# Kernel tuning notes

Measured on AMD Instinct MI355X. Metric: run time of the kernel, lower is better.

## Reference

```python
import jax, jax.numpy as jnp
from jax import lax
import numpy as np

B, C, N, T, K = 16, 64, 512, 64, 2
KSIZE, DIL = 2, 1
PAD = (KSIZE - 1) * DIL
EPS = 1e-5


def _powers(A, k):
    Ps = [jnp.eye(A.shape[0], dtype=A.dtype)]
    for _ in range(k):
        Ps.append(Ps[-1] @ A)
    return jnp.stack(Ps)  # (K+1, N, N)


def setup_inputs() -> dict:
    key = jax.random.key(0)
    ks = jax.random.split(key, 12)
    x = jax.random.normal(ks[0], (B, C, N, T), dtype=jnp.float32)
    # row-normalized random transition matrices, precomputed powers
    Af = jax.random.uniform(ks[1], (N, N), dtype=jnp.float32)
    Af = Af / Af.sum(axis=1, keepdims=True)
    Ab = Af.T / Af.T.sum(axis=1, keepdims=True)
    Aa = jax.random.uniform(ks[2], (N, N), dtype=jnp.float32)
    Aa = Aa / Aa.sum(axis=1, keepdims=True)
    P_f_pows = _powers(Af, K)
    P_b_pows = _powers(Ab, K)
    A_adp_pows = _powers(Aa, K)
    s = 0.05
    filter_w = jax.random.normal(ks[3], (C, C, 1, KSIZE), dtype=jnp.float32) * s
    filter_b = jnp.zeros((C,), jnp.float32)
    gate_w = jax.random.normal(ks[4], (C, C, 1, KSIZE), dtype=jnp.float32) * s
    gate_b = jnp.zeros((C,), jnp.float32)
    skip_w = jax.random.normal(ks[5], (C, C, 1, 1), dtype=jnp.float32) * s
    skip_b = jnp.zeros((C,), jnp.float32)
    weight_f = jax.random.normal(ks[6], (K + 1, C, C), dtype=jnp.float32) * s
    weight_b = jax.random.normal(ks[7], (K + 1, C, C), dtype=jnp.float32) * s
    gcn_bias = jnp.zeros((C,), jnp.float32)
    ln_gamma = jnp.ones((C,), jnp.float32)
    ln_beta = jnp.zeros((C,), jnp.float32)
    alpha = jnp.float32(0.5)
    return dict(x=x, P_f_pows=P_f_pows, P_b_pows=P_b_pows, A_adp_pows=A_adp_pows,
                filter_w=filter_w, filter_b=filter_b, gate_w=gate_w, gate_b=gate_b,
                skip_w=skip_w, skip_b=skip_b, weight_f=weight_f, weight_b=weight_b,
                gcn_bias=gcn_bias, ln_gamma=ln_gamma, ln_beta=ln_beta, alpha=alpha)


def _conv(x, w, b, dil=1):
    y = lax.conv_general_dilated(x, w, window_strides=(1, 1), padding='VALID',
                                 rhs_dilation=(1, dil),
                                 dimension_numbers=('NCHW', 'OIHW', 'NCHW'))
    return y + b[None, :, None, None]


def _apply_powers(xt, P_pows, weights):
    # xt: (B*T, N, Cin); P_pows: (K+1, N, N); weights: (K+1, Cin, Cout)
    xk = jnp.einsum('kij,bjc->kbic', P_pows, xt)
    return jnp.einsum('kbic,kco->bio', xk, weights)


def reference(x, P_f_pows, P_b_pows, A_adp_pows,
              filter_w, filter_b, gate_w, gate_b, skip_w, skip_b,
              weight_f, weight_b, gcn_bias, ln_gamma, ln_beta, alpha):
    # --- Gated TCN (causal left-pad along time) ---
    x_pad = jnp.pad(x, ((0, 0), (0, 0), (0, 0), (PAD, 0)))
    f = jnp.tanh(_conv(x_pad, filter_w, filter_b, DIL))
    g = jax.nn.sigmoid(_conv(x_pad, gate_w, gate_b, DIL))
    out = f * g                                   # (B, C, N, T)
    skip = _conv(out, skip_w, skip_b)             # 1x1 conv
    x_temporal = x + out                          # in_channels == out_channels

    # --- Diffusion GCN on (B*T, N, C) ---
    xt = jnp.transpose(x_temporal, (0, 3, 2, 1)).reshape(B * T, N, C)
    static_out = (_apply_powers(xt, P_f_pows, weight_f)
                  + _apply_powers(xt, P_b_pows, weight_b)
                  + gcn_bias[None, None, :])
    adapt_out = (_apply_powers(xt, A_adp_pows, weight_f)
                 + _apply_powers(xt, A_adp_pows, weight_b)
                 + gcn_bias[None, None, :])

    a = jax.nn.sigmoid(alpha)
    x_gcn = a * static_out + (1.0 - a) * adapt_out

    # --- LayerNorm over channel dim (dropout = identity in eval) ---
    mu = x_gcn.mean(axis=-1, keepdims=True)
    var = ((x_gcn - mu) ** 2).mean(axis=-1, keepdims=True)
    x_gcn = (x_gcn - mu) * lax.rsqrt(var + EPS) * ln_gamma + ln_beta

    x_out = x_gcn.reshape(B, T, N, C).transpose(0, 3, 2, 1)  # (B, C, N, T)
    return (x_out, skip)
```

## Files before the change

kernel.cpp:

```cpp
#include <hip/hip_runtime.h>
#include <cstdint>
#include <cstddef>

#define NB 16
#define NC 64
#define NN 512
#define NT 64
#define BT (NB*NT)
#define NN2 (NN*NN)
#define XSTRIDE_B (NC*NN*NT)
#define XSTRIDE_C (NN*NT)
#define XT_ROW (BT*NC)

typedef __attribute__((ext_vector_type(8))) short short8;
typedef __attribute__((ext_vector_type(4))) float f32x4;
typedef unsigned short ushort_t;
typedef unsigned int uint_t;

__device__ __forceinline__ ushort_t f2bf(float f) {
    uint_t u = __builtin_bit_cast(uint_t, f);
    u += 0x7FFFu + ((u >> 16) & 1u);
    return (ushort_t)(u >> 16);
}
__device__ __forceinline__ float bf2f(ushort_t u) {
    return __builtin_bit_cast(float, (uint_t)u << 16);
}
__device__ __forceinline__ void gl_lds16(const void* g, void* s) {
    __builtin_amdgcn_global_load_lds(
        (const __attribute__((address_space(1))) unsigned int*)g,
        (__attribute__((address_space(3))) unsigned int*)s, 16, 0, 0);
}
__device__ __forceinline__ void wait_vm(int n) {
    if (n >= 7)      asm volatile("s_waitcnt vmcnt(7)" ::: "memory");
    else if (n == 5) asm volatile("s_waitcnt vmcnt(5)" ::: "memory");
    else if (n == 4) asm volatile("s_waitcnt vmcnt(4)" ::: "memory");
    else if (n == 3) asm volatile("s_waitcnt vmcnt(3)" ::: "memory");
    else if (n == 2) asm volatile("s_waitcnt vmcnt(2)" ::: "memory");
    else             asm volatile("s_waitcnt vmcnt(0)" ::: "memory");
}

__global__ void k_prep(const float* __restrict__ wf, const float* __restrict__ wb,
                       const float* __restrict__ alpha, ushort_t* __restrict__ Wcb) {
    int i = blockIdx.x * 256 + threadIdx.x;
    if (i >= 7 * 4096) return;
    float a = 1.f / (1.f + expf(-alpha[0]));
    int r = i >> 12, co = i & 4095;
    int c = co >> 6, o = co & 63;
    float v;
    if      (r == 0) v = wf[co] + wb[co];
    else if (r == 1) v = a * wf[4096 + co];
    else if (r == 2) v = a * wf[8192 + co];
    else if (r == 3) v = a * wb[4096 + co];
    else if (r == 4) v = a * wb[8192 + co];
    else if (r == 5) v = (1.f - a) * (wf[4096 + co] + wb[4096 + co]);
    else             v = (1.f - a) * (wf[8192 + co] + wb[8192 + co]);
    int chunk = ((c >> 5) << 2) | (o >> 4);
    int lane  = (((c >> 3) & 3) << 4) | (o & 15);
    int j     = c & 7;
    Wcb[r * 4096 + chunk * 512 + lane * 8 + j] = f2bf(v);
}

__global__ void k_prepP(const float* __restrict__ Pf, const float* __restrict__ Pb,
                        const float* __restrict__ Aa, ushort_t* __restrict__ Apk) {
    int i = blockIdx.x * 256 + threadIdx.x;
    if (i >= 196608) return;
    int lane = i & 63, kc = (i >> 6) & 15, nt = (i >> 10) & 31, r = i >> 15;
    const float* base;
    if      (r == 0) base = Pf + NN2;
    else if (r == 1) base = Pf + 2 * NN2;
    else if (r == 2) base = Pb + NN2;
    else if (r == 3) base = Pb + 2 * NN2;
    else if (r == 4) base = Aa + NN2;
    else             base = Aa + 2 * NN2;
    int n = nt * 16 + (lane & 15);
    int k0 = kc * 32 + (lane >> 4) * 8;
    const float* src = base + (size_t)n * NN + k0;
    float4 v0 = ((const float4*)src)[0];
    float4 v1 = ((const float4*)src)[1];
    uint4 o;
    o.x = (uint_t)f2bf(v0.x) | ((uint_t)f2bf(v0.y) << 16);
    o.y = (uint_t)f2bf(v0.z) | ((uint_t)f2bf(v0.w) << 16);
    o.z = (uint_t)f2bf(v1.x) | ((uint_t)f2bf(v1.y) << 16);
    o.w = (uint_t)f2bf(v1.z) | ((uint_t)f2bf(v1.w) << 16);
    *(uint4*)(Apk + (size_t)i * 8) = o;
}

__global__ void k_prepW(const float* __restrict__ fw, const float* __restrict__ gw,
                        const float* __restrict__ sw, ushort_t* __restrict__ Wt) {
    int i = blockIdx.x * 256 + threadIdx.x;
    if (i >= 5 * 4096) return;
    int mat = i >> 12, t = i & 4095;
    int chunk = t >> 9, l = (t >> 3) & 63, j = t & 7;
    int m = chunk >> 1, kb = chunk & 1;
    int o = m * 16 + (l & 15);
    int c = kb * 32 + ((l >> 4) << 3) + j;
    float v;
    if      (mat == 0) v = fw[o * 128 + c * 2 + 0];
    else if (mat == 1) v = fw[o * 128 + c * 2 + 1];
    else if (mat == 2) v = gw[o * 128 + c * 2 + 0];
    else if (mat == 3) v = gw[o * 128 + c * 2 + 1];
    else               v = sw[o * 64 + c];
    Wt[i] = f2bf(v);
}

#define XS_P 72
__device__ __forceinline__ int swzA(int r, int c) {
    return r * XS_P + (c ^ (((r >> 4) & 3) << 3));
}
__global__ __launch_bounds__(256, 3) void k_tcn(
    const float* __restrict__ x,
    const ushort_t* __restrict__ Wt,
    const float* __restrict__ fb, const float* __restrict__ gb,
    const float* __restrict__ sb,
    float* __restrict__ skip_out, ushort_t* __restrict__ XTbf) {
    __shared__ __align__(16) ushort_t Xs[65 * XS_P];
    __shared__ __align__(16) ushort_t Os[64 * XS_P];

    int tx = threadIdx.x;
    int b = blockIdx.x >> 9, n = blockIdx.x & (NN - 1);

    {
        int c = tx >> 2, tq = tx & 3, t0 = tq * 16;
        const float* src = x + (size_t)b * XSTRIDE_B + (size_t)c * XSTRIDE_C
                             + (size_t)n * NT + t0;
        float4 v0 = ((const float4*)src)[0];
        float4 v1 = ((const float4*)src)[1];
        float4 v2 = ((const float4*)src)[2];
        float4 v3 = ((const float4*)src)[3];
        float vv[16] = {v0.x, v0.y, v0.z, v0.w, v1.x, v1.y, v1.z, v1.w,
                        v2.x, v2.y, v2.z, v2.w, v3.x, v3.y, v3.z, v3.w};
#pragma unroll
        for (int e = 0; e < 16; ++e) {
            int r = t0 + e + 1;
            Xs[swzA(r, c)] = f2bf(vv[e]);
        }
        if (tx < 8) ((uint4*)Xs)[tx] = (uint4){0, 0, 0, 0};
    }
    __syncthreads();

    int w = tx >> 6, l = tx & 63, lr = l & 15, lg = l >> 4;

    short8 wf0[2], wf1[2], wg0[2], wg1[2], wsk[2];
#pragma unroll
    for (int kb = 0; kb < 2; ++kb) {
        int off = (w * 2 + kb) * 512 + l * 8;
        wf0[kb] = *(const short8*)(Wt + 0 * 4096 + off);
        wf1[kb] = *(const short8*)(Wt + 1 * 4096 + off);
        wg0[kb] = *(const short8*)(Wt + 2 * 4096 + off);
        wg1[kb] = *(const short8*)(Wt + 3 * 4096 + off);
        wsk[kb] = *(const short8*)(Wt + 4 * 4096 + off);
    }
    float fbv[4], gbv[4], sbv[4];
#pragma unroll
    for (int q = 0; q < 4; ++q) {
        int o = w * 16 + lg * 4 + q;
        fbv[q] = fb[o]; gbv[q] = gb[o]; sbv[q] = sb[o];
    }

#pragma unroll
    for (int tb = 0; tb < 4; ++tb) {
        short8 b0[2], b1[2];
#pragma unroll
        for (int kb = 0; kb < 2; ++kb) {
            int blk = kb * 4 + lg;
            int r1 = tb * 16 + lr + 1, r0 = tb * 16 + lr;
            b1[kb] = *(const short8*)&Xs[r1 * XS_P + (((blk ^ ((r1 >> 4) & 3)) << 3))];
            b0[kb] = *(const short8*)&Xs[r0 * XS_P + (((blk ^ ((r0 >> 4) & 3)) << 3))];
        }
        f32x4 aF = {fbv[0], fbv[1], fbv[2], fbv[3]};
        f32x4 aG = {gbv[0], gbv[1], gbv[2], gbv[3]};
        aF = __builtin_amdgcn_mfma_f32_16x16x32_bf16(wf0[0], b0[0], aF, 0, 0, 0);
        aF = __builtin_amdgcn_mfma_f32_16x16x32_bf16(wf0[1], b0[1], aF, 0, 0, 0);
        aF = __builtin_amdgcn_mfma_f32_16x16x32_bf16(wf1[0], b1[0], aF, 0, 0, 0);
        aF = __builtin_amdgcn_mfma_f32_16x16x32_bf16(wf1[1], b1[1], aF, 0, 0, 0);
        aG = __builtin_amdgcn_mfma_f32_16x16x32_bf16(wg0[0], b0[0], aG, 0, 0, 0);
        aG = __builtin_amdgcn_mfma_f32_16x16x32_bf16(wg0[1], b0[1], aG, 0, 0, 0);
        aG = __builtin_amdgcn_mfma_f32_16x16x32_bf16(wg1[0], b1[0], aG, 0, 0, 0);
        aG = __builtin_amdgcn_mfma_f32_16x16x32_bf16(wg1[1], b1[1], aG, 0, 0, 0);
        int t = tb * 16 + lr;
#pragma unroll
        for (int q = 0; q < 4; ++q) {
            float fo = tanhf(aF[q]);
            float go = 1.f / (1.f + expf(-aG[q]));
            int o = w * 16 + lg * 4 + q;
            Os[swzA(t, o)] = f2bf(fo * go);
        }
    }
    __syncthreads();

    float* skp = skip_out + (size_t)b * XSTRIDE_B + (size_t)n * NT;
#pragma unroll
    for (int tb = 0; tb < 4; ++tb) {
        int t = tb * 16 + lr;
        short8 ov[2];
#pragma unroll
        for (int kb = 0; kb < 2; ++kb) {
            int blk = kb * 4 + lg;
            ov[kb] = *(const short8*)&Os[t * XS_P + (((blk ^ ((t >> 4) & 3)) << 3))];
        }
        f32x4 aS = {sbv[0], sbv[1], sbv[2], sbv[3]};
        aS = __builtin_amdgcn_mfma_f32_16x16x32_bf16(wsk[0], ov[0], aS, 0, 0, 0);
        aS = __builtin_amdgcn_mfma_f32_16x16x32_bf16(wsk[1], ov[1], aS, 0, 0, 0);
#pragma unroll
        for (int q = 0; q < 4; ++q) {
            int o = w * 16 + lg * 4 + q;
            skp[(size_t)o * XSTRIDE_C + t] = aS[q];
        }
    }

    {
        int t = tx >> 2, cch = (tx & 3) * 16;
        ushort_t* dst = XTbf + (size_t)n * XT_ROW + (size_t)b * 4096 + t * 64 + cch;
        int rX = t + 1;
#pragma unroll
        for (int blk2 = 0; blk2 < 2; ++blk2) {
            int cb = (cch >> 3) + blk2;
            short8 xv = *(const short8*)&Xs[rX * XS_P + ((cb ^ ((rX >> 4) & 3)) << 3)];
            short8 ovv = *(const short8*)&Os[t * XS_P + ((cb ^ ((t >> 4) & 3)) << 3)];
            uint_t pk[4];
#pragma unroll
            for (int h = 0; h < 4; ++h) {
                float s0 = bf2f((ushort_t)xv[h * 2]) + bf2f((ushort_t)ovv[h * 2]);
                float s1 = bf2f((ushort_t)xv[h * 2 + 1]) + bf2f((ushort_t)ovv[h * 2 + 1]);
                pk[h] = (uint_t)f2bf(s0) | ((uint_t)f2bf(s1) << 16);
            }
            *(uint4*)(dst + blk2 * 8) = (uint4){pk[0], pk[1], pk[2], pk[3]};
        }
    }
}

__global__ __launch_bounds__(256) void k_tr(const ushort_t* __restrict__ XTbf,
                                            ushort_t* __restrict__ Bpk) {
    __shared__ ushort_t tile[32 * XS_P];
    int tx = threadIdx.x;
    int bt = blockIdx.x;
    int jj = tx >> 3, c8 = (tx & 7) * 8;
    int f = tx >> 6, lane = tx & 63, lg = lane >> 4, lr = lane & 15;
    for (int kc = 0; kc < 16; ++kc) {
        if (kc) __syncthreads();
        *(uint4*)&tile[jj * XS_P + c8] =
            *(const uint4*)(XTbf + (size_t)(kc * 32 + jj) * XT_ROW + bt * 64 + c8);
        __syncthreads();
        ushort_t vals[8];
#pragma unroll
        for (int e = 0; e < 8; ++e)
            vals[e] = tile[(lg * 8 + e) * XS_P + f * 16 + lr];
        uint4 o;
        o.x = (uint_t)vals[0] | ((uint_t)vals[1] << 16);
        o.y = (uint_t)vals[2] | ((uint_t)vals[3] << 16);
        o.z = (uint_t)vals[4] | ((uint_t)vals[5] << 16);
        o.w = (uint_t)vals[6] | ((uint_t)vals[7] << 16);
        *(uint4*)(Bpk + (size_t)bt * 32768 + kc * 2048 + tx * 8) = o;
    }
}

__global__ __launch_bounds__(256, 4) void k_gcn(
    const ushort_t* __restrict__ Apk,
    const ushort_t* __restrict__ Bpk,
    const ushort_t* __restrict__ XTbf,
    const ushort_t* __restrict__ Wcb,
    const float* __restrict__ bias,
    ushort_t* __restrict__ G) {
    __shared__ __align__(16) char smem[24576];

    int tx = threadIdx.x;
    int w = tx >> 6, l = tx & 63;
    int lr = l & 15, lg = l >> 4;
    int s = w >> 1, h = w & 1;

    int bid = (blockIdx.x & 7) * 2048 + (blockIdx.x >> 3);
    int bt = bid >> 4;
    int n0i = bid & 15;
    int n0 = n0i << 5;

    f32x4 acc[3][4];
#pragma unroll
    for (int j = 0; j < 3; ++j)
#pragma unroll
        for (int f = 0; f < 4; ++f) acc[j][f] = (f32x4){0.f, 0.f, 0.f, 0.f};

    const ushort_t* aBase = Apk + (size_t)(h * 3) * NN2
                                + (size_t)(n0i * 2 + s) * 8192 + l * 8;
    const ushort_t* a2Src = aBase + 2 * (size_t)NN2;
    const ushort_t* bSrc = Bpk + (size_t)bt * 32768 + w * 512 + l * 8;

    short8 aE[2], aO[2];
    aE[0] = *(const short8*)(aBase);
    aE[1] = *(const short8*)(aBase + NN2);
#pragma unroll
    for (int d = 0; d < 2; ++d)
        gl_lds16(a2Src + d * 512, smem + 16384 + d * 4096 + w * 1024);
#pragma unroll
    for (int d = 0; d < 3; ++d)
        gl_lds16(bSrc + d * 2048, smem + d * 4096 + w * 1024);
    wait_vm(2);
    __builtin_amdgcn_s_barrier();
    __builtin_amdgcn_sched_barrier(0);

#pragma unroll
    for (int t = 0; t < 16; ++t) {
        if (t + 1 < 16) {
            if ((t & 1) == 0) {
                aO[0] = *(const short8*)(aBase + (t + 1) * 512);
                aO[1] = *(const short8*)(aBase + NN2 + (t + 1) * 512);
            } else {
                aE[0] = *(const short8*)(aBase + (t + 1) * 512);
                aE[1] = *(const short8*)(aBase + NN2 + (t + 1) * 512);
            }
        }
        if (t + 2 < 16)
            gl_lds16(a2Src + (t + 2) * 512,
                     smem + 16384 + ((t + 2) & 1) * 4096 + w * 1024);
        if (t + 3 < 16)
            gl_lds16(bSrc + (t + 3) * 2048,
                     smem + ((t + 3) & 3) * 4096 + w * 1024);

        const char* sBr = smem + (t & 3) * 4096;
        short8 a2 = *(const short8*)(smem + 16384 + (t & 1) * 4096 + w * 1024 + l * 16);
        short8 bv[4];
#pragma unroll
        for (int f = 0; f < 4; ++f)
            bv[f] = *(const short8*)(sBr + f * 1024 + l * 16);

        __builtin_amdgcn_s_setprio(1);
        const short8 a0 = (t & 1) ? aO[0] : aE[0];
        const short8 a1 = (t & 1) ? aO[1] : aE[1];
#pragma unroll
        for (int f = 0; f < 4; ++f)
            acc[0][f] = __builtin_amdgcn_mfma_f32_16x16x32_bf16(a0, bv[f], acc[0][f], 0, 0, 0);
#pragma unroll
        for (int f = 0; f < 4; ++f)
            acc[1][f] = __builtin_amdgcn_mfma_f32_16x16x32_bf16(a1, bv[f], acc[1][f], 0, 0, 0);
#pragma unroll
        for (int f = 0; f < 4; ++f)
            acc[2][f] = __builtin_amdgcn_mfma_f32_16x16x32_bf16(a2, bv[f], acc[2][f], 0, 0, 0);
        __builtin_amdgcn_s_setprio(0);

        wait_vm(t <= 12 ? 5 : (t == 13 ? 4 : (t == 14 ? 2 : 0)));
        __builtin_amdgcn_s_barrier();
        __builtin_amdgcn_sched_barrier(0);
    }

    float* sC = (float*)smem;
    ushort_t* sYw = (ushort_t*)(smem + 8192) + w * 1152;

    f32x4 acc2[4];
#pragma unroll
    for (int fo = 0; fo < 4; ++fo) {
        float b = (h == 0) ? bias[fo * 16 + lr] : 0.f;
        acc2[fo] = (f32x4){b, b, b, b};
    }
    const ushort_t* wBase = Wcb + l * 8;

    if (h == 0) {
        const ushort_t* xs = XTbf + (size_t)(n0 + s * 16 + lr) * XT_ROW + bt * 64 + lg * 8;
        short8 ay0 = *(const short8*)(xs);
        short8 ay1 = *(const short8*)(xs + 32);
#pragma unroll
        for (int kh = 0; kh < 2; ++kh)
#pragma unroll
            for (int fo = 0; fo < 4; ++fo) {
                short8 wv = *(const short8*)(wBase + (kh * 4 + fo) * 512);
                acc2[fo] = __builtin_amdgcn_mfma_f32_16x16x32_bf16(
                    kh ? ay1 : ay0, wv, acc2[fo], 0, 0, 0);
            }
    }
#pragma unroll
    for (int j = 0; j < 3; ++j) {
        int wcIdx = (h == 0) ? (j + 1) : (j + 4);
#pragma unroll
        for (int f = 0; f < 4; ++f)
#pragma unroll
            for (int q = 0; q < 4; ++q)
                sYw[(lg * 4 + q) * 72 + f * 16 + lr] = f2bf(acc[j][f][q]);
        short8 ay0 = *(const short8*)(&sYw[lr * 72 + lg * 8]);
        short8 ay1 = *(const short8*)(&sYw[lr * 72 + 32 + lg * 8]);
#pragma unroll
        for (int kh = 0; kh < 2; ++kh)
#pragma unroll
            for (int fo = 0; fo < 4; ++fo) {
                short8 wv = *(const short8*)(wBase + wcIdx * 4096 + (kh * 4 + fo) * 512);
                acc2[fo] = __builtin_amdgcn_mfma_f32_16x16x32_bf16(
                    kh ? ay1 : ay0, wv, acc2[fo], 0, 0, 0);
            }
    }

    if (h == 1) {
#pragma unroll
        for (int fo = 0; fo < 4; ++fo)
            *(f32x4*)&sC[(s * 4 + fo) * 256 + l * 4] = acc2[fo];
    }
    __syncthreads();
    if (h == 0) {
        ushort_t* gp = G + (size_t)(n0 + s * 16 + lg * 4) * XT_ROW + bt * 64 + lr;
#pragma unroll
        for (int fo = 0; fo < 4; ++fo) {
            f32x4 other = *(const f32x4*)&sC[(s * 4 + fo) * 256 + l * 4];
#pragma unroll
            for (int q = 0; q < 4; ++q)
                gp[(size_t)q * XT_ROW + fo * 16] = f2bf(acc2[fo][q] + other[q]);
        }
    }
}

__global__ __launch_bounds__(256) void k_ln_t(
    const ushort_t* __restrict__ G,
    const float* __restrict__ gamma, const float* __restrict__ beta,
    float* __restrict__ xout) {
    __shared__ float sT[64 * 65];
    __shared__ float sMu[64], sRs[64];
    __shared__ float sS[64 * 4], sQ[64 * 4];

    int bid = blockIdx.x;
    int b = bid >> 9, n = bid & (NN - 1);
    int tx = threadIdx.x;
    const ushort_t* src = G + (size_t)n * XT_ROW + (size_t)b * (NT * NC);

#pragma unroll
    for (int u = 0; u < 2; ++u) {
        int fi = u * 256 + tx;
        uint4 v = ((const uint4*)src)[fi];
        int t = fi >> 3, c = (fi & 7) * 8;
        sT[t * 65 + c + 0] = bf2f((ushort_t)(v.x & 0xffff));
        sT[t * 65 + c + 1] = bf2f((ushort_t)(v.x >> 16));
        sT[t * 65 + c + 2] = bf2f((ushort_t)(v.y & 0xffff));
        sT[t * 65 + c + 3] = bf2f((ushort_t)(v.y >> 16));
        sT[t * 65 + c + 4] = bf2f((ushort_t)(v.z & 0xffff));
        sT[t * 65 + c + 5] = bf2f((ushort_t)(v.z >> 16));
        sT[t * 65 + c + 6] = bf2f((ushort_t)(v.w & 0xffff));
        sT[t * 65 + c + 7] = bf2f((ushort_t)(v.w >> 16));
    }
    __syncthreads();
    {
        int row = tx >> 2, seg = tx & 3;
        float s = 0.f, q = 0.f;
        for (int cc = 0; cc < 16; ++cc) {
            float v = sT[row * 65 + seg * 16 + cc];
            s += v; q += v * v;
        }
        sS[row * 4 + seg] = s; sQ[row * 4 + seg] = q;
    }
    __syncthreads();
    if (tx < 64) {
        float ss = sS[tx * 4] + sS[tx * 4 + 1] + sS[tx * 4 + 2] + sS[tx * 4 + 3];
        float qq = sQ[tx * 4] + sQ[tx * 4 + 1] + sQ[tx * 4 + 2] + sQ[tx * 4 + 3];
        float mu = ss * (1.f / 64.f);
        float var = qq * (1.f / 64.f) - mu * mu;
        sMu[tx] = mu; sRs[tx] = rsqrtf(var + 1e-5f);
    }
    __syncthreads();
    {
        int t = tx & 63, cg = (tx >> 6) * 16;
        float mu = sMu[t], rs = sRs[t];
        for (int cc = 0; cc < 16; ++cc) {
            int c = cg + cc;
            float v = (sT[t * 65 + c] - mu) * rs * gamma[c] + beta[c];
            xout[(size_t)b * XSTRIDE_B + (size_t)c * XSTRIDE_C + (size_t)n * NT + t] = v;
        }
    }
}

extern "C" void kernel_launch(void* const* d_in, const int* in_sizes, int n_in,
                              void* d_out, int out_size, void* d_ws, size_t ws_size,
                              hipStream_t stream) {
    const float* x     = (const float*)d_in[0];
    const float* Pf    = (const float*)d_in[1];
    const float* Pb    = (const float*)d_in[2];
    const float* Aa    = (const float*)d_in[3];
    const float* fw    = (const float*)d_in[4];
    const float* fb    = (const float*)d_in[5];
    const float* gw    = (const float*)d_in[6];
    const float* gb    = (const float*)d_in[7];
    const float* sw    = (const float*)d_in[8];
    const float* sb    = (const float*)d_in[9];
    const float* wf    = (const float*)d_in[10];
    const float* wb    = (const float*)d_in[11];
    const float* gbias = (const float*)d_in[12];
    const float* lng   = (const float*)d_in[13];
    const float* lnb   = (const float*)d_in[14];
    const float* alpha = (const float*)d_in[15];

    float* xout = (float*)d_out;
    float* skip = (float*)d_out + (size_t)NB * NC * NN * NT;

    char* ws = (char*)d_ws;
    ushort_t* XTbf = (ushort_t*)(ws);
    ushort_t* Bpk  = (ushort_t*)(ws + 67108864);
    ushort_t* Gb   = (ushort_t*)(ws + 134217728);
    ushort_t* Apk  = (ushort_t*)(ws + 201326592);
    ushort_t* Wcb  = (ushort_t*)(ws + 204472320);
    ushort_t* Wt   = (ushort_t*)(ws + 204537856);

    hipLaunchKernelGGL(k_prep, dim3(112), dim3(256), 0, stream, wf, wb, alpha, Wcb);
    hipLaunchKernelGGL(k_prepW, dim3(80), dim3(256), 0, stream, fw, gw, sw, Wt);
    hipLaunchKernelGGL(k_prepP, dim3(768), dim3(256), 0, stream, Pf, Pb, Aa, Apk);
    hipLaunchKernelGGL(k_tcn, dim3(NB * NN), dim3(256), 0, stream,
                       x, Wt, fb, gb, sb, skip, XTbf);
    hipLaunchKernelGGL(k_tr, dim3(1024), dim3(256), 0, stream, XTbf, Bpk);
    hipLaunchKernelGGL(k_gcn, dim3(16384), dim3(256), 0, stream,
                       Apk, Bpk, XTbf, Wcb, gbias, Gb);
    hipLaunchKernelGGL(k_ln_t, dim3(NB * NN), dim3(256), 0, stream, Gb, lng, lnb, xout);
}
```

Baseline: 402.4 us.

## Stream all A operands via registers and halve barriers with 2-step pipeline

The GCN main loop previously staged the third A-power operand through LDS and synchronized every k-step. It now loads all three A fragments directly into registers, and it processes two k-steps per iteration with a 6-slot B ring buffer prefetched four steps ahead, which halves the number of barriers. The vmcnt wait thresholds are retuned to match the new load counts. The change frees LDS and cuts synchronisation, at the cost of more VGPRs for the extra A fragments and a deeper prefetch, which could reduce occupancy.

```diff
diff --git a/kernel.cpp b/kernel.cpp
--- a/kernel.cpp
+++ b/kernel.cpp
@@ -31,10 +31,9 @@
         (__attribute__((address_space(3))) unsigned int*)s, 16, 0, 0);
 }
 __device__ __forceinline__ void wait_vm(int n) {
-    if (n >= 7)      asm volatile("s_waitcnt vmcnt(7)" ::: "memory");
-    else if (n == 5) asm volatile("s_waitcnt vmcnt(5)" ::: "memory");
+    if (n >= 8)      asm volatile("s_waitcnt vmcnt(8)" ::: "memory");
+    else if (n == 6) asm volatile("s_waitcnt vmcnt(6)" ::: "memory");
     else if (n == 4) asm volatile("s_waitcnt vmcnt(4)" ::: "memory");
-    else if (n == 3) asm volatile("s_waitcnt vmcnt(3)" ::: "memory");
     else if (n == 2) asm volatile("s_waitcnt vmcnt(2)" ::: "memory");
     else             asm volatile("s_waitcnt vmcnt(0)" ::: "memory");
 }
@@ -281,62 +280,80 @@
 
     const ushort_t* aBase = Apk + (size_t)(h * 3) * NN2
                                 + (size_t)(n0i * 2 + s) * 8192 + l * 8;
-    const ushort_t* a2Src = aBase + 2 * (size_t)NN2;
     const ushort_t* bSrc = Bpk + (size_t)bt * 32768 + w * 512 + l * 8;
 
-    short8 aE[2], aO[2];
-    aE[0] = *(const short8*)(aBase);
-    aE[1] = *(const short8*)(aBase + NN2);
-#pragma unroll
-    for (int d = 0; d < 2; ++d)
-        gl_lds16(a2Src + d * 512, smem + 16384 + d * 4096 + w * 1024);
-#pragma unroll
-    for (int d = 0; d < 3; ++d)
+    short8 aA0[3], aA1[3], aB[3];
+#pragma unroll
+    for (int j = 0; j < 3; ++j) aA0[j] = *(const short8*)(aBase + (size_t)j * NN2);
+#pragma unroll
+    for (int d = 0; d < 4; ++d)
         gl_lds16(bSrc + d * 2048, smem + d * 4096 + w * 1024);
     wait_vm(2);
     __builtin_amdgcn_s_barrier();
     __builtin_amdgcn_sched_barrier(0);
 
 #pragma unroll
-    for (int t = 0; t < 16; ++t) {
-        if (t + 1 < 16) {
-            if ((t & 1) == 0) {
-                aO[0] = *(const short8*)(aBase + (t + 1) * 512);
-                aO[1] = *(const short8*)(aBase + NN2 + (t + 1) * 512);
+    for (int g = 0; g < 8; ++g) {
+        const int k0 = 2 * g, k1 = 2 * g + 1;
+#pragma unroll
+        for (int j = 0; j < 3; ++j)
+            aB[j] = *(const short8*)(aBase + (size_t)j * NN2 + k1 * 512);
+        if (k0 + 2 < 16) {
+            if ((g & 1) == 0) {
+#pragma unroll
+                for (int j = 0; j < 3; ++j)
+                    aA1[j] = *(const short8*)(aBase + (size_t)j * NN2 + (k0 + 2) * 512);
             } else {
-                aE[0] = *(const short8*)(aBase + (t + 1) * 512);
-                aE[1] = *(const short8*)(aBase + NN2 + (t + 1) * 512);
+#pragma unroll
+                for (int j = 0; j < 3; ++j)
+                    aA0[j] = *(const short8*)(aBase + (size_t)j * NN2 + (k0 + 2) * 512);
             }
         }
-        if (t + 2 < 16)
-            gl_lds16(a2Src + (t + 2) * 512,
-                     smem + 16384 + ((t + 2) & 1) * 4096 + w * 1024);
-        if (t + 3 < 16)
-            gl_lds16(bSrc + (t + 3) * 2048,
-                     smem + ((t + 3) & 3) * 4096 + w * 1024);
-
-        const char* sBr = smem + (t & 3) * 4096;
-        short8 a2 = *(const short8*)(smem + 16384 + (t & 1) * 4096 + w * 1024 + l * 16);
-        short8 bv[4];
-#pragma unroll
-        for (int f = 0; f < 4; ++f)
-            bv[f] = *(const short8*)(sBr + f * 1024 + l * 16);
-
-        __builtin_amdgcn_s_setprio(1);
-        const short8 a0 = (t & 1) ? aO[0] : aE[0];
-        const short8 a1 = (t & 1) ? aO[1] : aE[1];
-#pragma unroll
-        for (int f = 0; f < 4; ++f)
-            acc[0][f] = __builtin_amdgcn_mfma_f32_16x16x32_bf16(a0, bv[f], acc[0][f], 0, 0, 0);
-#pragma unroll
-        for (int f = 0; f < 4; ++f)
-            acc[1][f] = __builtin_amdgcn_mfma_f32_16x16x32_bf16(a1, bv[f], acc[1][f], 0, 0, 0);
-#pragma unroll
-        for (int f = 0; f < 4; ++f)
-            acc[2][f] = __builtin_amdgcn_mfma_f32_16x16x32_bf16(a2, bv[f], acc[2][f], 0, 0, 0);
-        __builtin_amdgcn_s_setprio(0);
-
-        wait_vm(t <= 12 ? 5 : (t == 13 ? 4 : (t == 14 ? 2 : 0)));
+        if (k0 + 4 < 16)
+            gl_lds16(bSrc + (k0 + 4) * 2048, smem + ((k0 + 4) % 6) * 4096 + w * 1024);
+        if (k1 + 4 < 16)
+            gl_lds16(bSrc + (k1 + 4) * 2048, smem + ((k1 + 4) % 6) * 4096 + w * 1024);
+
+        {
+            const char* sBr = smem + (k0 % 6) * 4096;
+            short8 bv[4];
+#pragma unroll
+            for (int f = 0; f < 4; ++f)
+                bv[f] = *(const short8*)(sBr + f * 1024 + l * 16);
+            const short8 a0 = (g & 1) ? aA1[0] : aA0[0];
+            const short8 a1 = (g & 1) ? aA1[1] : aA0[1];
+            const short8 a2 = (g & 1) ? aA1[2] : aA0[2];
+            __builtin_amdgcn_s_setprio(1);
+#pragma unroll
+            for (int f = 0; f < 4; ++f)
+                acc[0][f] = __builtin_amdgcn_mfma_f32_16x16x32_bf16(a0, bv[f], acc[0][f], 0, 0, 0);
+#pragma unroll
+            for (int f = 0; f < 4; ++f)
+                acc[1][f] = __builtin_amdgcn_mfma_f32_16x16x32_bf16(a1, bv[f], acc[1][f], 0, 0, 0);
+#pragma unroll
+            for (int f = 0; f < 4; ++f)
+                acc[2][f] = __builtin_amdgcn_mfma_f32_16x16x32_bf16(a2, bv[f], acc[2][f], 0, 0, 0);
+            __builtin_amdgcn_s_setprio(0);
+        }
+        {
+            const char* sBr = smem + (k1 % 6) * 4096;
+            short8 bv[4];
+#pragma unroll
+            for (int f = 0; f < 4; ++f)
+                bv[f] = *(const short8*)(sBr + f * 1024 + l * 16);
+            __builtin_amdgcn_s_setprio(1);
+#pragma unroll
+            for (int f = 0; f < 4; ++f)
+                acc[0][f] = __builtin_amdgcn_mfma_f32_16x16x32_bf16(aB[0], bv[f], acc[0][f], 0, 0, 0);
+#pragma unroll
+            for (int f = 0; f < 4; ++f)
+                acc[1][f] = __builtin_amdgcn_mfma_f32_16x16x32_bf16(aB[1], bv[f], acc[1][f], 0, 0, 0);
+#pragma unroll
+            for (int f = 0; f < 4; ++f)
+                acc[2][f] = __builtin_amdgcn_mfma_f32_16x16x32_bf16(aB[2], bv[f], acc[2][f], 0, 0, 0);
+            __builtin_amdgcn_s_setprio(0);
+        }
+        wait_vm(g <= 5 ? 8 : (g == 6 ? 6 : 0));
         __builtin_amdgcn_s_barrier();
         __builtin_amdgcn_sched_barrier(0);
     }
```

Measured after the change: 392.2 us, median of 2. -2.5%, faster.
